# Kernel optimization log

Hardware: AMD Instinct MI355X
Metric: run time of the kernel (lower is better)

The kernel has to match this reference:

```python
import jax, jax.numpy as jnp
import numpy as np

NUM_CLASSES = 80
PRE_NMS_K = 400    # pre_nms_points / max_output_size_per_class
MAX_BOXES = 200    # max_total_size
NMS_THRESH = 0.6
SCORE_THRESH = 0.0  # iou_thresh in YoloLayer, used as score threshold/mask
SCALE_XY = (1.2, 1.1, 1.05)  # levels 3,4,5
STRIDES = (8.0, 16.0, 32.0)  # 2**level


def setup_inputs() -> dict:
    key = jax.random.key(0)
    k3, k4, k5 = jax.random.split(key, 3)
    B, C5 = 8, 3 * (NUM_CLASSES + 5)
    p3 = jax.random.normal(k3, (B, 64, 64, C5), dtype=jnp.float32)
    p4 = jax.random.normal(k4, (B, 32, 32, C5), dtype=jnp.float32)
    p5 = jax.random.normal(k5, (B, 16, 16, C5), dtype=jnp.float32)
    a3 = jnp.array([[12., 16.], [19., 36.], [40., 28.]], jnp.float32)
    a4 = jnp.array([[36., 75.], [76., 55.], [72., 146.]], jnp.float32)
    a5 = jnp.array([[142., 110.], [192., 243.], [459., 401.]], jnp.float32)
    return {"p3": p3, "p4": p4, "p5": p5, "a3": a3, "a4": a4, "a5": a5}


def _decode_level(p, anchors, stride, scale_xy):
    # p: [B,H,W,A*(C+5)] raw head output; 'original' box decode (sigmoid xy, exp wh)
    B, H, W, _ = p.shape
    A = anchors.shape[0]
    d = p.reshape(B, H, W, A, NUM_CLASSES + 5)
    txy, twh, tobj, tcls = d[..., :2], d[..., 2:4], d[..., 4:5], d[..., 5:]
    gx, gy = jnp.meshgrid(jnp.arange(W, dtype=p.dtype), jnp.arange(H, dtype=p.dtype))
    grid = jnp.stack([gx, gy], -1)[None, :, :, None, :]          # [1,H,W,1,2] (x,y)
    sxy = jnp.asarray(scale_xy, p.dtype)
    xy = (jax.nn.sigmoid(txy) * sxy - 0.5 * (sxy - 1.0) + grid) / jnp.array([W, H], p.dtype)
    wh = jnp.exp(twh) * anchors[None, None, None] / jnp.array([W * stride, H * stride], p.dtype)
    x1y1 = xy - 0.5 * wh
    x2y2 = xy + 0.5 * wh
    boxes = jnp.stack([x1y1[..., 1], x1y1[..., 0], x2y2[..., 1], x2y2[..., 0]], -1)  # yxyx
    obj = jax.nn.sigmoid(tobj)
    cls = jax.nn.sigmoid(tcls) * obj
    N = H * W * A
    return boxes.reshape(B, N, 4), cls.reshape(B, N, NUM_CLASSES), obj.reshape(B, N)


def _pairwise_iou(b):
    # b: [K,4] yxyx in [0,1]
    area = (b[:, 2] - b[:, 0]) * (b[:, 3] - b[:, 1])
    tl = jnp.maximum(b[:, None, :2], b[None, :, :2])
    br = jnp.minimum(b[:, None, 2:], b[None, :, 2:])
    wh = jnp.maximum(br - tl, 0.0)
    inter = wh[..., 0] * wh[..., 1]
    union = area[:, None] + area[None, :] - inter
    return inter / jnp.maximum(union, 1e-9)


def _greedy_nms_scores(boxes, scores):
    # boxes/scores already sorted by score descending; returns scores with suppressed -> 0
    K = scores.shape[0]
    overlap = _pairwise_iou(boxes) > NMS_THRESH
    idx = jnp.arange(K)

    def body(i, keep):
        sup = overlap[i] & (idx > i) & keep[i]
        return keep & ~sup

    keep = jax.lax.fori_loop(0, K, body, jnp.ones((K,), bool))
    return jnp.where(keep & (scores > SCORE_THRESH), scores, 0.0)


def _detections_per_image(boxes, cls_scores):
    # boxes [N,4], cls_scores [N,C] -> combined per-class NMS, top MAX_BOXES overall
    boxes = jnp.clip(boxes, 0.0, 1.0)  # combined NMS clips boxes by default

    def per_class(scores_c):
        vals, idx = jax.lax.top_k(scores_c, PRE_NMS_K)
        b = boxes[idx]
        return _greedy_nms_scores(b, vals), b

    kept_scores, kept_boxes = jax.vmap(per_class)(cls_scores.T)  # [C,K], [C,K,4]
    flat_s = kept_scores.reshape(-1)
    flat_b = kept_boxes.reshape(-1, 4)
    cls_ids = jnp.repeat(jnp.arange(NUM_CLASSES), PRE_NMS_K)
    top_s, top_i = jax.lax.top_k(flat_s, MAX_BOXES)
    top_b = flat_b[top_i]
    top_c = cls_ids[top_i].astype(jnp.float32)
    valid = top_s > 0.0
    top_b = jnp.where(valid[:, None], top_b, 0.0)
    top_c = jnp.where(valid, top_c, 0.0)
    num = jnp.sum(valid.astype(jnp.int32))
    return top_b, top_s, top_c, num


def _forward(p3, p4, p5, a3, a4, a5):
    boxes, cls_scores, obj_scores = [], [], []
    for (p, a), stride, sxy in zip(((p3, a3), (p4, a4), (p5, a5)), STRIDES, SCALE_XY):
        b, c, o = _decode_level(p, a, stride, sxy)
        boxes.append(b); cls_scores.append(c); obj_scores.append(o)
    boxes = jnp.concatenate(boxes, 1)            # [B,N,4]
    cls_scores = jnp.concatenate(cls_scores, 1)  # [B,N,C]
    obj_scores = jnp.concatenate(obj_scores, 1)  # [B,N]
    obj_mask = (obj_scores > SCORE_THRESH).astype(boxes.dtype)
    cls_mask = (cls_scores > SCORE_THRESH).astype(boxes.dtype)
    cls_scores = cls_scores * obj_mask[..., None] * cls_mask
    return jax.vmap(_detections_per_image)(boxes, cls_scores)


def reference(p3, p4, p5, a3, a4, a5):
    bbox, confidence, classes, num_detections = _forward(p3, p4, p5, a3, a4, a5)
    return bbox, confidence, classes, num_detections
```

## Files before the change

### kernel.cpp

```cpp
#include <hip/hip_runtime.h>
#include <math.h>

#define NCLS 80
#define PRE_K 400
#define MAX_BOXES 200
#define KEEP_CAP 200
#define N_TOT 16128
#define M_FIN (NCLS * KEEP_CAP)
#define NMS_T 0.6f
#define NTHR 512
#define CAP 512

typedef unsigned long long u64;
typedef unsigned int u32;
typedef unsigned short u16;

__device__ __forceinline__ float sigf(float x) { return 1.0f / (1.0f + expf(-x)); }

__device__ __forceinline__ float score_f32(int idx, int b, int c,
    const float* __restrict__ p3, const float* __restrict__ p4, const float* __restrict__ p5)
{
    const float* base; int W, n;
    if (idx < 12288)      { base = p3; W = 64; n = idx; }
    else if (idx < 15360) { base = p4; W = 32; n = idx - 12288; }
    else                  { base = p5; W = 16; n = idx - 15360; }
    int a = n % 3, hw = n / 3, w = hw % W, h = hw / W;
    const float* rec = base + (((b * W + h) * W + w) * 255 + a * 85);
    return sigf(rec[5 + c]) * sigf(rec[4]);
}

__device__ __forceinline__ void hist_agg(u32* hist, u32 d, bool valid, int lane)
{
    u64 act = __ballot(valid);
    while (act) {
        int ldr = __ffsll((unsigned long long)act) - 1;
        u32 dl = __shfl(d, ldr, 64);
        u64 m = __ballot(valid && d == dl);
        if (lane == ldr) atomicAdd(&hist[dl], (u32)__popcll(m));
        act &= ~m;
    }
}

__device__ __forceinline__ void digit_select(const u32* hist, int need,
                                             u32* sh_dg, u32* sh_S1, u32* sh_T, int tid)
{
    if (tid < 64) {
        const int lane = tid;
        u32 h0 = hist[4 * lane + 0], h1 = hist[4 * lane + 1];
        u32 h2 = hist[4 * lane + 2], h3 = hist[4 * lane + 3];
        u32 loc = h0 + h1 + h2 + h3;
        u32 s = loc;
#pragma unroll
        for (int off = 1; off < 64; off <<= 1) {
            u32 t = __shfl_down(s, off, 64);
            if (lane + off < 64) s += t;
        }
        u32 after = s - loc;
        u32 S3 = h3 + after, S2 = h2 + S3, S1v = h1 + S2, S0 = h0 + S1v;
        u32 Sarr[5] = { S0, S1v, S2, S3, after };
#pragma unroll
        for (int k = 0; k < 4; ++k) {
            if ((int)Sarr[k] >= need && need > (int)Sarr[k + 1]) {
                *sh_dg = (u32)(4 * lane + k);
                *sh_S1 = Sarr[k + 1];
                *sh_T  = Sarr[k] - Sarr[k + 1];
            }
        }
    }
    __syncthreads();
}

__device__ __forceinline__ void sort512(u64* cand, int tid)
{
    u64 v = cand[tid];
#pragma unroll
    for (int k2 = 2; k2 <= 64; k2 <<= 1) {
#pragma unroll
        for (int j = k2 >> 1; j > 0; j >>= 1) {
            u64 p = __shfl_xor(v, j, 64);
            bool takeMax = ((tid & k2) == 0) ^ ((tid & j) != 0);
            v = takeMax ? (v >= p ? v : p) : (v <= p ? v : p);
        }
    }
    for (int k2 = 128; k2 <= CAP; k2 <<= 1) {
        for (int j = k2 >> 1; j >= 64; j >>= 1) {
            __syncthreads();
            cand[tid] = v;
            __syncthreads();
            u64 p = cand[tid ^ j];
            bool takeMax = ((tid & k2) == 0) ^ ((tid & j) != 0);
            v = takeMax ? (v >= p ? v : p) : (v <= p ? v : p);
        }
#pragma unroll
        for (int j = 32; j > 0; j >>= 1) {
            u64 p = __shfl_xor(v, j, 64);
            bool takeMax = ((tid & k2) == 0) ^ ((tid & j) != 0);
            v = takeMax ? (v >= p ? v : p) : (v <= p ? v : p);
        }
    }
    __syncthreads();
    cand[tid] = v;
    __syncthreads();
}

__global__ __launch_bounds__(256) void decode_kernel(
    const float* __restrict__ p3, const float* __restrict__ p4, const float* __restrict__ p5,
    const float* __restrict__ a3, const float* __restrict__ a4, const float* __restrict__ a5,
    u16* __restrict__ scores16, float* __restrict__ boxes)
{
    const int blk = blockIdx.x;
    const int b = blk & 7;
    const int n = ((blk >> 3) << 8) + threadIdx.x;

    const float* base; const float* anc; int logw, nn; float sx;
    if (n < 12288)      { base = p3; anc = a3; logw = 6; nn = n;         sx = 1.2f;  }
    else if (n < 15360) { base = p4; anc = a4; logw = 5; nn = n - 12288; sx = 1.1f;  }
    else                { base = p5; anc = a5; logw = 4; nn = n - 15360; sx = 1.05f; }
    const int W = 1 << logw;
    const int a = nn % 3; const int hw = nn / 3;
    const int w = hw & (W - 1); const int h = hw >> logw;
    const float winv = 1.0f / (float)W;
    const float* rec = base + ((size_t)((b * W + h) * W + w) * 255 + a * 85);

    float tx = rec[0], ty = rec[1], tw = rec[2], th = rec[3], to = rec[4];
    float sobj = sigf(to);
    float cx = (sigf(tx) * sx - 0.5f * (sx - 1.0f) + (float)w) * winv;
    float cy = (sigf(ty) * sx - 0.5f * (sx - 1.0f) + (float)h) * winv;
    float bw = expf(tw) * anc[a * 2 + 0] * (1.0f / 512.0f);
    float bh = expf(th) * anc[a * 2 + 1] * (1.0f / 512.0f);
    float x1 = cx - 0.5f * bw, x2 = cx + 0.5f * bw;
    float y1 = cy - 0.5f * bh, y2 = cy + 0.5f * bh;
    y1 = fminf(fmaxf(y1, 0.f), 1.f); x1 = fminf(fmaxf(x1, 0.f), 1.f);
    y2 = fminf(fmaxf(y2, 0.f), 1.f); x2 = fminf(fmaxf(x2, 0.f), 1.f);
    float4 bb; bb.x = y1; bb.y = x1; bb.z = y2; bb.w = x2;
    ((float4*)boxes)[b * N_TOT + n] = bb;

    u16* sb = scores16 + (long)b * NCLS * N_TOT + n;
#pragma unroll 8
    for (int cc = 0; cc < NCLS; ++cc)
        sb[(long)cc * N_TOT] = (u16)(__float_as_uint(sigf(rec[5 + cc]) * sobj) >> 16);
}

__global__ __launch_bounds__(NTHR, 6) void topk_nms_fused(
    const u16* __restrict__ scores16, const float* __restrict__ boxes,
    const float* __restrict__ p3, const float* __restrict__ p4, const float* __restrict__ p5,
    float* __restrict__ ksc, float* __restrict__ kbox)
{
    __shared__ alignas(16) u64 cand[CAP];
    __shared__ u32 hist[260];
    __shared__ u32 sh_dg, sh_S1, sh_T;
    __shared__ int sh_gcnt;
    __shared__ alignas(16) float boxbuf[5 * 448];
    __shared__ alignas(16) u64 supc[64 * 7];
    __shared__ u64 keepw[7];
    __shared__ int wpre[8];
    __shared__ int sh_ncnt;

    float* by1 = boxbuf;
    float* bx1 = boxbuf + 448;
    float* by2 = boxbuf + 896;
    float* bx2 = boxbuf + 1344;
    float* bar = boxbuf + 1792;

    const int tid = threadIdx.x;
    const int wv = tid >> 6;
    const int lane = tid & 63;
    const int b = blockIdx.x & 7;
    const int c = blockIdx.x >> 3;

    const u16* keys16 = scores16 + (long)(b * NCLS + c) * N_TOT;
    const uint4* k4 = (const uint4*)keys16;
    const int N8 = N_TOT >> 3;

    if (tid < 260) hist[tid] = 0u;
    if (tid == 0) sh_gcnt = 0;
    __syncthreads();
#pragma unroll
    for (int it = 0; it < 4; ++it) {
        int i4 = tid + it * NTHR;
        bool v = i4 < N8;
        u32 e0 = 0, e1 = 0, e2 = 0, e3 = 0, e4 = 0, e5 = 0, e6 = 0, e7 = 0;
        if (v) {
            uint4 kk = k4[i4];
            e0 = kk.x & 0xffffu; e1 = kk.x >> 16; e2 = kk.y & 0xffffu; e3 = kk.y >> 16;
            e4 = kk.z & 0xffffu; e5 = kk.z >> 16; e6 = kk.w & 0xffffu; e7 = kk.w >> 16;
        }
        hist_agg(hist, e0 >> 8, v, lane); hist_agg(hist, e1 >> 8, v, lane);
        hist_agg(hist, e2 >> 8, v, lane); hist_agg(hist, e3 >> 8, v, lane);
        hist_agg(hist, e4 >> 8, v, lane); hist_agg(hist, e5 >> 8, v, lane);
        hist_agg(hist, e6 >> 8, v, lane); hist_agg(hist, e7 >> 8, v, lane);
    }
    __syncthreads();

    int need = PRE_K;
    digit_select(hist, need, &sh_dg, &sh_S1, &sh_T, tid);
    u32 thr = sh_dg; need -= (int)sh_S1;
    int C = (PRE_K - need) + (int)sh_T;
    int lvl = 1;

    if (C > CAP) {
        if (tid < 256) hist[tid] = 0u;
        __syncthreads();
#pragma unroll
        for (int it = 0; it < 4; ++it) {
            int i4 = tid + it * NTHR;
            if (i4 < N8) {
                uint4 kk = k4[i4];
                u32 e[8] = { kk.x & 0xffffu, kk.x >> 16, kk.y & 0xffffu, kk.y >> 16,
                             kk.z & 0xffffu, kk.z >> 16, kk.w & 0xffffu, kk.w >> 16 };
#pragma unroll
                for (int q = 0; q < 8; ++q)
                    if ((e[q] >> 8) == thr) atomicAdd(&hist[e[q] & 255u], 1u);
            }
        }
        __syncthreads();
        digit_select(hist, need, &sh_dg, &sh_S1, &sh_T, tid);
        thr = (thr << 8) | sh_dg; need -= (int)sh_S1;
        C = (PRE_K - need) + (int)sh_T;
        lvl = 2;
    }

    if (C > CAP) {
        u32 t16 = thr;
        if (tid < 256) hist[tid] = 0u;
        __syncthreads();
        for (int i = tid; i < N_TOT; i += NTHR) {
            if (keys16[i] == (u16)t16) {
                u32 kb = __float_as_uint(score_f32(i, b, c, p3, p4, p5));
                atomicAdd(&hist[(kb >> 8) & 255u], 1u);
            }
        }
        __syncthreads();
        digit_select(hist, need, &sh_dg, &sh_S1, &sh_T, tid);
        thr = (thr << 8) | sh_dg; need -= (int)sh_S1;
        C = (PRE_K - need) + (int)sh_T;
        lvl = 3;
    }

    if (C > CAP) {
        u32 t16 = thr >> 8;
        if (tid < 256) hist[tid] = 0u;
        __syncthreads();
        for (int i = tid; i < N_TOT; i += NTHR) {
            if (keys16[i] == (u16)t16) {
                u32 kb = __float_as_uint(score_f32(i, b, c, p3, p4, p5));
                if ((kb >> 8) == thr) atomicAdd(&hist[kb & 255u], 1u);
            }
        }
        __syncthreads();
        digit_select(hist, need, &sh_dg, &sh_S1, &sh_T, tid);
        thr = (thr << 8) | sh_dg; need -= (int)sh_S1;
        C = (PRE_K - need) + (int)sh_T;
        lvl = 4;
    }

    if (lvl <= 2) {
#pragma unroll
        for (int it = 0; it < 4; ++it) {
            int i4 = tid + it * NTHR;
            if (i4 < N8) {
                uint4 kk = k4[i4];
                int i0 = i4 << 3;
                u32 e[8] = { kk.x & 0xffffu, kk.x >> 16, kk.y & 0xffffu, kk.y >> 16,
                             kk.z & 0xffffu, kk.z >> 16, kk.w & 0xffffu, kk.w >> 16 };
#pragma unroll
                for (int q = 0; q < 8; ++q) {
                    bool take = (lvl == 1) ? ((e[q] >> 8) >= thr) : (e[q] >= thr);
                    if (take) {
                        int p = atomicAdd(&sh_gcnt, 1);
                        int i = i0 + q;
                        u32 kb = __float_as_uint(score_f32(i, b, c, p3, p4, p5));
                        cand[p] = ((u64)kb << 32) | (u32)(0xFFFFFFFFu - (u32)i);
                    }
                }
            }
        }
        __syncthreads();
        for (int t = C + tid; t < CAP; t += NTHR) cand[t] = 0ull;
    } else if (C <= CAP) {
        u32 t16 = (lvl == 3) ? (thr >> 8) : (thr >> 16);
        for (int i = tid; i < N_TOT; i += NTHR) {
            u32 k = keys16[i];
            bool take = false;
            u32 kb = 0;
            if (k > t16) { take = true; kb = __float_as_uint(score_f32(i, b, c, p3, p4, p5)); }
            else if (k == t16) {
                kb = __float_as_uint(score_f32(i, b, c, p3, p4, p5));
                take = (lvl == 3) ? ((kb >> 8) >= thr) : (kb >= thr);
            }
            if (take) {
                int p = atomicAdd(&sh_gcnt, 1);
                cand[p] = ((u64)kb << 32) | (u32)(0xFFFFFFFFu - (u32)i);
            }
        }
        __syncthreads();
        for (int t = C + tid; t < CAP; t += NTHR) cand[t] = 0ull;
    } else {
        u32 t16 = thr >> 16;
        for (int i = tid; i < N_TOT; i += NTHR) {
            u32 k = keys16[i];
            if (k < t16) continue;
            u32 kb = __float_as_uint(score_f32(i, b, c, p3, p4, p5));
            if (kb > thr) {
                int p = atomicAdd(&sh_gcnt, 1);
                cand[p] = ((u64)kb << 32) | (u32)(0xFFFFFFFFu - (u32)i);
            }
        }
        __syncthreads();
        const int G = sh_gcnt;
        u32* scr = (u32*)boxbuf;
        int lo = tid * 32; if (lo > N_TOT) lo = N_TOT;
        int hi = lo + 32;  if (hi > N_TOT) hi = N_TOT;
        int lc = 0;
        for (int i = lo; i < hi; ++i)
            if (keys16[i] == (u16)t16 &&
                __float_as_uint(score_f32(i, b, c, p3, p4, p5)) == thr) ++lc;
        u32* sc_cur = scr; u32* sc_oth = scr + 512;
        sc_cur[tid] = (u32)lc;
        __syncthreads();
        for (int off = 1; off < NTHR; off <<= 1) {
            sc_oth[tid] = sc_cur[tid] + ((tid >= off) ? sc_cur[tid - off] : 0u);
            __syncthreads();
            u32* tmp = sc_cur; sc_cur = sc_oth; sc_oth = tmp;
        }
        int r = (int)sc_cur[tid] - lc;
        for (int i = lo; i < hi; ++i) {
            if (keys16[i] == (u16)t16 &&
                __float_as_uint(score_f32(i, b, c, p3, p4, p5)) == thr) {
                if (r < need) cand[G + r] = ((u64)thr << 32) | (u32)(0xFFFFFFFFu - (u32)i);
                ++r;
            }
        }
        __syncthreads();
        for (int t = PRE_K + tid; t < CAP; t += NTHR) cand[t] = 0ull;
    }
    __syncthreads();

    sort512(cand, tid);

    const float4* btab = (const float4*)boxes;
    for (int t = tid; t < 448; t += NTHR) {
        float y1 = 0.f, x1 = 0.f, y2 = 0.f, x2 = 0.f;
        if (t < PRE_K) {
            u64 key = cand[t];
            if ((key >> 32) != 0ull) {
                int idx = (int)(0xFFFFFFFFu - (u32)(key & 0xFFFFFFFFull));
                float4 bb = btab[b * N_TOT + idx];
                y1 = bb.x; x1 = bb.y; y2 = bb.z; x2 = bb.w;
            }
        }
        by1[t] = y1; bx1[t] = x1; by2[t] = y2; bx2[t] = x2;
        bar[t] = (y2 - y1) * (x2 - x1);
    }
    if (tid < 7) keepw[tid] = (tid < 6) ? ~0ull : 0xFFFFull;
    __syncthreads();

    for (int ch = 0; ch < 7; ++ch) {
        const int rbase = ch << 6;
        const int nrows = (PRE_K - rbase < 64) ? (PRE_K - rbase) : 64;
        for (int r = wv; r < nrows; r += 8) {
            int row = rbase + r;
            if ((keepw[ch] >> r) & 1ull) {
                float ry1 = by1[row], rx1 = bx1[row], ry2 = by2[row], rx2 = bx2[row], ra = bar[row];
                for (int cw = ch; cw < 7; ++cw) {
                    int j = (cw << 6) + lane;
                    bool o = false;
                    if (j > row && j < PRE_K) {
                        float ty = fmaxf(ry1, by1[j]);
                        float tx = fmaxf(rx1, bx1[j]);
                        float by = fminf(ry2, by2[j]);
                        float rx = fminf(rx2, bx2[j]);
                        float hh = fmaxf(by - ty, 0.f);
                        float ww = fmaxf(rx - tx, 0.f);
                        float inter = hh * ww;
                        float uni = ra + bar[j] - inter;
                        o = (inter / fmaxf(uni, 1e-9f)) > NMS_T;
                    }
                    u64 m = __ballot(o);
                    if (lane == 0) supc[r * 7 + cw] = m;
                }
            }
        }
        __syncthreads();
        if (tid < 64) {
            u64 kw = (tid < 7) ? keepw[tid] : 0ull;
            u64 s_cur = (tid < 7) ? supc[tid] : 0ull;
            for (int r = 0; r < nrows; ++r) {
                u64 s_next = (tid < 7 && (r + 1) < nrows) ? supc[(r + 1) * 7 + tid] : 0ull;
                u64 kwv = __shfl(kw, ch);
                if (((kwv >> r) & 1ull) && tid >= ch) kw &= ~s_cur;
                s_cur = s_next;
            }
            if (tid < 7) keepw[tid] = kw;
        }
        __syncthreads();
    }

    if (tid == 0) {
        int acc = 0;
        for (int w = 0; w < 7; ++w) { wpre[w] = acc; acc += (int)__popcll(keepw[w]); }
        sh_ncnt = acc < KEEP_CAP ? acc : KEEP_CAP;
    }
    __syncthreads();

    const int blk_out = b * NCLS + c;
    float* osc = ksc + (long)blk_out * KEEP_CAP;
    float* obx = kbox + (long)blk_out * KEEP_CAP * 4;
    for (int t = tid; t < PRE_K; t += NTHR) {
        int w = t >> 6, bb = t & 63;
        u64 kwv = keepw[w];
        if ((kwv >> bb) & 1ull) {
            int pos = wpre[w] + (int)__popcll(kwv & ((1ull << bb) - 1ull));
            if (pos < KEEP_CAP) {
                osc[pos] = __uint_as_float((u32)(cand[t] >> 32));
                obx[pos * 4 + 0] = by1[t]; obx[pos * 4 + 1] = bx1[t];
                obx[pos * 4 + 2] = by2[t]; obx[pos * 4 + 3] = bx2[t];
            }
        }
    }
    for (int t = sh_ncnt + tid; t < KEEP_CAP; t += NTHR) {
        osc[t] = 0.0f;
        obx[t * 4 + 0] = 0.f; obx[t * 4 + 1] = 0.f;
        obx[t * 4 + 2] = 0.f; obx[t * 4 + 3] = 0.f;
    }
}

__device__ __forceinline__ void radix_topk_sort_f32(
    const u32* __restrict__ keys, int n, int K,
    u64* cand, u32* hist, u32* scr,
    u32* sh_dg, u32* sh_S1, u32* sh_T, int* sh_gcnt, int tid)
{
    int need = K;
    digit_select(hist, need, sh_dg, sh_S1, sh_T, tid);
    u32 thr = *sh_dg; need -= (int)*sh_S1;
    int C = (K - need) + (int)*sh_T;
    int eshift = 24;

    const uint4* k4 = (const uint4*)keys;
    const int n4 = n >> 2;
    const int nIter = (n4 + NTHR - 1) / NTHR;

    for (int shift = 16; shift >= 0 && C > CAP; shift -= 8) {
        if (tid < 256) hist[tid] = 0u;
        __syncthreads();
        for (int it = 0; it < nIter; ++it) {
            int i4 = tid + it * NTHR;
            if (i4 < n4) {
                uint4 kk = k4[i4];
                if ((kk.x >> (shift + 8)) == thr) atomicAdd(&hist[(kk.x >> shift) & 255u], 1u);
                if ((kk.y >> (shift + 8)) == thr) atomicAdd(&hist[(kk.y >> shift) & 255u], 1u);
                if ((kk.z >> (shift + 8)) == thr) atomicAdd(&hist[(kk.z >> shift) & 255u], 1u);
                if ((kk.w >> (shift + 8)) == thr) atomicAdd(&hist[(kk.w >> shift) & 255u], 1u);
            }
        }
        __syncthreads();
        digit_select(hist, need, sh_dg, sh_S1, sh_T, tid);
        thr = (thr << 8) | *sh_dg; need -= (int)*sh_S1;
        C = (K - need) + (int)*sh_T;
        eshift = shift;
    }

    if (C <= CAP) {
        for (int it = 0; it < nIter; ++it) {
            int i4 = tid + it * NTHR;
            if (i4 < n4) {
                uint4 kk = k4[i4];
                int i0 = i4 << 2;
                if ((kk.x >> eshift) >= thr) { int p = atomicAdd(sh_gcnt, 1); cand[p] = ((u64)kk.x << 32) | (u32)(0xFFFFFFFFu - (u32)(i0 + 0)); }
                if ((kk.y >> eshift) >= thr) { int p = atomicAdd(sh_gcnt, 1); cand[p] = ((u64)kk.y << 32) | (u32)(0xFFFFFFFFu - (u32)(i0 + 1)); }
                if ((kk.z >> eshift) >= thr) { int p = atomicAdd(sh_gcnt, 1); cand[p] = ((u64)kk.z << 32) | (u32)(0xFFFFFFFFu - (u32)(i0 + 2)); }
                if ((kk.w >> eshift) >= thr) { int p = atomicAdd(sh_gcnt, 1); cand[p] = ((u64)kk.w << 32) | (u32)(0xFFFFFFFFu - (u32)(i0 + 3)); }
            }
        }
        __syncthreads();
        for (int t = C + tid; t < CAP; t += NTHR) cand[t] = 0ull;
    } else {
        for (int i = tid; i < n; i += NTHR) {
            u32 k = keys[i];
            if (k > thr) {
                int p = atomicAdd(sh_gcnt, 1);
                cand[p] = ((u64)k << 32) | (u32)(0xFFFFFFFFu - (u32)i);
            }
        }
        __syncthreads();
        const int G = *sh_gcnt;
        int lo = tid * 32; if (lo > n) lo = n;
        int hi = lo + 32;  if (hi > n) hi = n;
        int lc = 0;
        for (int i = lo; i < hi; ++i) if (keys[i] == thr) ++lc;
        u32* sc_cur = scr; u32* sc_oth = scr + 512;
        sc_cur[tid] = (u32)lc;
        __syncthreads();
        for (int off = 1; off < NTHR; off <<= 1) {
            sc_oth[tid] = sc_cur[tid] + ((tid >= off) ? sc_cur[tid - off] : 0u);
            __syncthreads();
            u32* tmp = sc_cur; sc_cur = sc_oth; sc_oth = tmp;
        }
        int r = (int)sc_cur[tid] - lc;
        for (int i = lo; i < hi; ++i) {
            if (keys[i] == thr) {
                if (r < need) cand[G + r] = ((u64)thr << 32) | (u32)(0xFFFFFFFFu - (u32)i);
                ++r;
            }
        }
        __syncthreads();
        for (int t = K + tid; t < CAP; t += NTHR) cand[t] = 0ull;
    }
    __syncthreads();
    sort512(cand, tid);
}

__global__ __launch_bounds__(NTHR) void final_topk_kernel(
    const float* __restrict__ ksc, const float* __restrict__ kbox,
    float* __restrict__ out)
{
    __shared__ alignas(16) u64 cand[CAP];
    __shared__ u32 hist[260];
    __shared__ u32 scr[1024];
    __shared__ u32 sh_dg, sh_S1, sh_T;
    __shared__ int sh_gcnt;

    const int tid = threadIdx.x;
    const int lane = tid & 63;
    const int b = blockIdx.x;
    const u32* keys = (const u32*)(ksc + (long)b * M_FIN);

    if (tid < 260) hist[tid] = 0u;
    if (tid == 0) sh_gcnt = 0;
    __syncthreads();
    const uint4* k4 = (const uint4*)keys;
#pragma unroll
    for (int it = 0; it < 8; ++it) {
        int i4 = tid + it * NTHR;
        bool v = i4 < (M_FIN >> 2);
        u32 d0 = 0, d1 = 0, d2 = 0, d3 = 0;
        if (v) {
            uint4 kk = k4[i4];
            d0 = kk.x >> 24; d1 = kk.y >> 24; d2 = kk.z >> 24; d3 = kk.w >> 24;
        }
        hist_agg(hist, d0, v, lane);
        hist_agg(hist, d1, v, lane);
        hist_agg(hist, d2, v, lane);
        hist_agg(hist, d3, v, lane);
    }
    __syncthreads();

    radix_topk_sort_f32(keys, M_FIN, MAX_BOXES, cand, hist, scr,
                        &sh_dg, &sh_S1, &sh_T, &sh_gcnt, tid);

    float* obb = out;
    float* ocf = out + 8 * MAX_BOXES * 4;
    float* ocl = ocf + 8 * MAX_BOXES;
    float* onm = ocl + 8 * MAX_BOXES;

    float s = 0.f;
    if (tid < MAX_BOXES) {
        u64 key = cand[tid];
        s = __uint_as_float((u32)(key >> 32));
        float y1 = 0.f, x1 = 0.f, y2 = 0.f, x2 = 0.f, cid = 0.f;
        if (s > 0.0f) {
            int i = (int)(0xFFFFFFFFu - (u32)(key & 0xFFFFFFFFull));
            int cc = i / KEEP_CAP, j = i % KEEP_CAP;
            const float* bb = kbox + (((long)b * NCLS + cc) * KEEP_CAP + j) * 4;
            y1 = bb[0]; x1 = bb[1]; y2 = bb[2]; x2 = bb[3];
            cid = (float)cc;
        }
        long o = (long)b * MAX_BOXES + tid;
        obb[o * 4 + 0] = y1; obb[o * 4 + 1] = x1; obb[o * 4 + 2] = y2; obb[o * 4 + 3] = x2;
        ocf[o] = s; ocl[o] = cid;
    }
    int cnt = __syncthreads_count(tid < MAX_BOXES && s > 0.0f);
    if (tid == 0) onm[b] = (float)cnt;
}

extern "C" void kernel_launch(void* const* d_in, const int* in_sizes, int n_in,
                              void* d_out, int out_size, void* d_ws, size_t ws_size,
                              hipStream_t stream) {
    const float* p3 = (const float*)d_in[0];
    const float* p4 = (const float*)d_in[1];
    const float* p5 = (const float*)d_in[2];
    const float* a3 = (const float*)d_in[3];
    const float* a4 = (const float*)d_in[4];
    const float* a5 = (const float*)d_in[5];
    float* out = (float*)d_out;

    const size_t s16_bytes  = (size_t)8 * NCLS * N_TOT * 2;
    const size_t box_bytes  = (size_t)8 * N_TOT * 16;
    const size_t ksc_bytes  = (size_t)8 * NCLS * KEEP_CAP * 4;

    u16*   scores16 = (u16*)d_ws;
    float* boxes    = (float*)((char*)d_ws + s16_bytes);
    float* ksc      = (float*)((char*)d_ws + s16_bytes + box_bytes);
    float* kbox     = (float*)((char*)d_ws + s16_bytes + box_bytes + ksc_bytes);

    decode_kernel<<<504, 256, 0, stream>>>(p3, p4, p5, a3, a4, a5, scores16, boxes);
    topk_nms_fused<<<8 * NCLS, NTHR, 0, stream>>>(scores16, boxes, p3, p4, p5, ksc, kbox);
    final_topk_kernel<<<8, NTHR, 0, stream>>>(ksc, kbox, out);
}
```

Measured before the change: 203.9 us.

## Cache score keys in LDS and restructure NMS into diagonal-block plus forward suppression

The 16-bit score keys for the block's class row are copied into shared memory during the first histogram pass, so later radix refinement and candidate-gather passes read LDS instead of global memory. The NMS is rewritten: each 64-row chunk first resolves suppression inside its diagonal block with a ballot loop, then only kept rows suppress later boxes, via per-column ballots and atomicAnd on a 32-bit keep bitmap. This skips IoU rows for already-suppressed boxes and removes the full suppression matrix. In exchange the 32 KB key buffer raises LDS use, so the launch bound drops from 6 to 4 blocks per SM, which lowers occupancy.

```diff
diff --git a/kernel.cpp b/kernel.cpp
--- a/kernel.cpp
+++ b/kernel.cpp
@@ -141,19 +141,21 @@
         sb[(long)cc * N_TOT] = (u16)(__float_as_uint(sigf(rec[5 + cc]) * sobj) >> 16);
 }
 
-__global__ __launch_bounds__(NTHR, 6) void topk_nms_fused(
+__global__ __launch_bounds__(NTHR, 4) void topk_nms_fused(
     const u16* __restrict__ scores16, const float* __restrict__ boxes,
     const float* __restrict__ p3, const float* __restrict__ p4, const float* __restrict__ p5,
     float* __restrict__ ksc, float* __restrict__ kbox)
 {
+    __shared__ alignas(16) u16 skey[N_TOT];
     __shared__ alignas(16) u64 cand[CAP];
     __shared__ u32 hist[260];
     __shared__ u32 sh_dg, sh_S1, sh_T;
     __shared__ int sh_gcnt;
     __shared__ alignas(16) float boxbuf[5 * 448];
-    __shared__ alignas(16) u64 supc[64 * 7];
-    __shared__ u64 keepw[7];
-    __shared__ int wpre[8];
+    __shared__ alignas(16) u64 diagbuf[64];
+    __shared__ u32 keepb[16];
+    __shared__ u64 sh_keptM;
+    __shared__ int wpre14[14];
     __shared__ int sh_ncnt;
 
     float* by1 = boxbuf;
@@ -168,8 +170,9 @@
     const int b = blockIdx.x & 7;
     const int c = blockIdx.x >> 3;
 
-    const u16* keys16 = scores16 + (long)(b * NCLS + c) * N_TOT;
-    const uint4* k4 = (const uint4*)keys16;
+    const u16* keys16g = scores16 + (long)(b * NCLS + c) * N_TOT;
+    const uint4* k4g = (const uint4*)keys16g;
+    const uint4* k4 = (const uint4*)skey;
     const int N8 = N_TOT >> 3;
 
     if (tid < 260) hist[tid] = 0u;
@@ -181,7 +184,8 @@
         bool v = i4 < N8;
         u32 e0 = 0, e1 = 0, e2 = 0, e3 = 0, e4 = 0, e5 = 0, e6 = 0, e7 = 0;
         if (v) {
-            uint4 kk = k4[i4];
+            uint4 kk = k4g[i4];
+            ((uint4*)skey)[i4] = kk;
             e0 = kk.x & 0xffffu; e1 = kk.x >> 16; e2 = kk.y & 0xffffu; e3 = kk.y >> 16;
             e4 = kk.z & 0xffffu; e5 = kk.z >> 16; e6 = kk.w & 0xffffu; e7 = kk.w >> 16;
         }
@@ -225,7 +229,7 @@
         if (tid < 256) hist[tid] = 0u;
         __syncthreads();
         for (int i = tid; i < N_TOT; i += NTHR) {
-            if (keys16[i] == (u16)t16) {
+            if (skey[i] == (u16)t16) {
                 u32 kb = __float_as_uint(score_f32(i, b, c, p3, p4, p5));
                 atomicAdd(&hist[(kb >> 8) & 255u], 1u);
             }
@@ -242,7 +246,7 @@
         if (tid < 256) hist[tid] = 0u;
         __syncthreads();
         for (int i = tid; i < N_TOT; i += NTHR) {
-            if (keys16[i] == (u16)t16) {
+            if (skey[i] == (u16)t16) {
                 u32 kb = __float_as_uint(score_f32(i, b, c, p3, p4, p5));
                 if ((kb >> 8) == thr) atomicAdd(&hist[kb & 255u], 1u);
             }
@@ -280,7 +284,7 @@
     } else if (C <= CAP) {
         u32 t16 = (lvl == 3) ? (thr >> 8) : (thr >> 16);
         for (int i = tid; i < N_TOT; i += NTHR) {
-            u32 k = keys16[i];
+            u32 k = skey[i];
             bool take = false;
             u32 kb = 0;
             if (k > t16) { take = true; kb = __float_as_uint(score_f32(i, b, c, p3, p4, p5)); }
@@ -298,7 +302,7 @@
     } else {
         u32 t16 = thr >> 16;
         for (int i = tid; i < N_TOT; i += NTHR) {
-            u32 k = keys16[i];
+            u32 k = skey[i];
             if (k < t16) continue;
             u32 kb = __float_as_uint(score_f32(i, b, c, p3, p4, p5));
             if (kb > thr) {
@@ -313,7 +317,7 @@
         int hi = lo + 32;  if (hi > N_TOT) hi = N_TOT;
         int lc = 0;
         for (int i = lo; i < hi; ++i)
-            if (keys16[i] == (u16)t16 &&
+            if (skey[i] == (u16)t16 &&
                 __float_as_uint(score_f32(i, b, c, p3, p4, p5)) == thr) ++lc;
         u32* sc_cur = scr; u32* sc_oth = scr + 512;
         sc_cur[tid] = (u32)lc;
@@ -325,7 +329,7 @@
         }
         int r = (int)sc_cur[tid] - lc;
         for (int i = lo; i < hi; ++i) {
-            if (keys16[i] == (u16)t16 &&
+            if (skey[i] == (u16)t16 &&
                 __float_as_uint(score_f32(i, b, c, p3, p4, p5)) == thr) {
                 if (r < need) cand[G + r] = ((u64)thr << 32) | (u32)(0xFFFFFFFFu - (u32)i);
                 ++r;
@@ -352,53 +356,77 @@
         by1[t] = y1; bx1[t] = x1; by2[t] = y2; bx2[t] = x2;
         bar[t] = (y2 - y1) * (x2 - x1);
     }
-    if (tid < 7) keepw[tid] = (tid < 6) ? ~0ull : 0xFFFFull;
+    if (tid < 16) keepb[tid] = (tid < 12) ? 0xFFFFFFFFu : ((tid == 12) ? 0xFFFFu : 0u);
     __syncthreads();
 
     for (int ch = 0; ch < 7; ++ch) {
         const int rbase = ch << 6;
-        const int nrows = (PRE_K - rbase < 64) ? (PRE_K - rbase) : 64;
-        for (int r = wv; r < nrows; r += 8) {
-            int row = rbase + r;
-            if ((keepw[ch] >> r) & 1ull) {
-                float ry1 = by1[row], rx1 = bx1[row], ry2 = by2[row], rx2 = bx2[row], ra = bar[row];
-                for (int cw = ch; cw < 7; ++cw) {
-                    int j = (cw << 6) + lane;
-                    bool o = false;
-                    if (j > row && j < PRE_K) {
-                        float ty = fmaxf(ry1, by1[j]);
-                        float tx = fmaxf(rx1, bx1[j]);
-                        float by = fminf(ry2, by2[j]);
-                        float rx = fminf(rx2, bx2[j]);
-                        float hh = fmaxf(by - ty, 0.f);
-                        float ww = fmaxf(rx - tx, 0.f);
-                        float inter = hh * ww;
-                        float uni = ra + bar[j] - inter;
-                        o = (inter / fmaxf(uni, 1e-9f)) > NMS_T;
+        const float ry1 = by1[rbase + lane], rx1v = bx1[rbase + lane];
+        const float ry2 = by2[rbase + lane], rx2v = bx2[rbase + lane];
+        const float ra  = bar[rbase + lane];
+
+#pragma unroll
+        for (int q = 0; q < 8; ++q) {
+            const int jl = wv * 8 + q;
+            const int jj = rbase + jl;
+            u64 m = 0ull;
+            if (jj < PRE_K && ((keepb[jj >> 5] >> (jj & 31)) & 1u)) {
+                float cy1 = by1[jj], cx1 = bx1[jj], cy2 = by2[jj], cx2 = bx2[jj], ca = bar[jj];
+                float ty = fmaxf(ry1, cy1), tx = fmaxf(rx1v, cx1);
+                float byv = fminf(ry2, cy2), rxv = fminf(rx2v, cx2);
+                float inter = fmaxf(byv - ty, 0.f) * fmaxf(rxv - tx, 0.f);
+                float uni = ra + ca - inter;
+                bool o = (lane < jl) && ((inter / fmaxf(uni, 1e-9f)) > NMS_T);
+                m = __ballot(o);
+            }
+            if (lane == 0) diagbuf[jl] = m;
+        }
+        __syncthreads();
+
+        if (tid < 64) {
+            u64 dg = diagbuf[lane];
+            int ri = rbase + lane;
+            int alive = (ri < PRE_K) ? (int)((keepb[ri >> 5] >> (ri & 31)) & 1u) : 0;
+            u64 M = __ballot(alive != 0);
+            for (int i = 0; i < 64; ++i) {
+                if ((M >> i) & 1ull) {
+                    int kill = (int)((dg >> i) & 1ull);
+                    alive &= ~kill;
+                    M = __ballot(alive != 0);
+                }
+            }
+            if (lane == 0) {
+                sh_keptM = M;
+                keepb[2 * ch]     = (u32)(M & 0xFFFFFFFFull);
+                keepb[2 * ch + 1] = (u32)(M >> 32);
+            }
+        }
+        __syncthreads();
+
+        {
+            const u64 keptM = sh_keptM;
+            if (keptM != 0ull) {
+                for (int jj = rbase + 64 + wv; jj < PRE_K; jj += 8) {
+                    if ((keepb[jj >> 5] >> (jj & 31)) & 1u) {
+                        float cy1 = by1[jj], cx1 = bx1[jj], cy2 = by2[jj], cx2 = bx2[jj], ca = bar[jj];
+                        float ty = fmaxf(ry1, cy1), tx = fmaxf(rx1v, cx1);
+                        float byv = fminf(ry2, cy2), rxv = fminf(rx2v, cx2);
+                        float inter = fmaxf(byv - ty, 0.f) * fmaxf(rxv - tx, 0.f);
+                        float uni = ra + ca - inter;
+                        bool o = (inter / fmaxf(uni, 1e-9f)) > NMS_T;
+                        u64 m = __ballot(o);
+                        if ((m & keptM) != 0ull && lane == 0)
+                            atomicAnd(&keepb[jj >> 5], ~(1u << (jj & 31)));
                     }
-                    u64 m = __ballot(o);
-                    if (lane == 0) supc[r * 7 + cw] = m;
                 }
             }
-        }
-        __syncthreads();
-        if (tid < 64) {
-            u64 kw = (tid < 7) ? keepw[tid] : 0ull;
-            u64 s_cur = (tid < 7) ? supc[tid] : 0ull;
-            for (int r = 0; r < nrows; ++r) {
-                u64 s_next = (tid < 7 && (r + 1) < nrows) ? supc[(r + 1) * 7 + tid] : 0ull;
-                u64 kwv = __shfl(kw, ch);
-                if (((kwv >> r) & 1ull) && tid >= ch) kw &= ~s_cur;
-                s_cur = s_next;
-            }
-            if (tid < 7) keepw[tid] = kw;
         }
         __syncthreads();
     }
 
     if (tid == 0) {
         int acc = 0;
-        for (int w = 0; w < 7; ++w) { wpre[w] = acc; acc += (int)__popcll(keepw[w]); }
+        for (int w = 0; w < 14; ++w) { wpre14[w] = acc; acc += __popc(keepb[w]); }
         sh_ncnt = acc < KEEP_CAP ? acc : KEEP_CAP;
     }
     __syncthreads();
@@ -407,10 +435,9 @@
     float* osc = ksc + (long)blk_out * KEEP_CAP;
     float* obx = kbox + (long)blk_out * KEEP_CAP * 4;
     for (int t = tid; t < PRE_K; t += NTHR) {
-        int w = t >> 6, bb = t & 63;
-        u64 kwv = keepw[w];
-        if ((kwv >> bb) & 1ull) {
-            int pos = wpre[w] + (int)__popcll(kwv & ((1ull << bb) - 1ull));
+        u32 kw = keepb[t >> 5];
+        if ((kw >> (t & 31)) & 1u) {
+            int pos = wpre14[t >> 5] + __popc(kw & ((1u << (t & 31)) - 1u));
             if (pos < KEEP_CAP) {
                 osc[pos] = __uint_as_float((u32)(cand[t] >> 32));
                 obx[pos * 4 + 0] = by1[t]; obx[pos * 4 + 1] = bx1[t];
```

New measurement: 169.0 us (median of 4 runs). 17.1% less time.
